# Performance work log

Measured on AMD Instinct MI355X. Metric: run time of the kernel, lower is better.

The kernel has to match this reference:

```python
import jax, jax.numpy as jnp
import numpy as np

B, L, D = 16, 512, 128
EPS = 1e-12


def _newton_schulz_1(S):
    # One Newton-Schulz orthogonalization iteration on batched [B,D,D] matrices:
    # X = S/||S||_F ; X <- 1.5*X - 0.5 * X @ X^T @ X
    norm = jnp.sqrt(jnp.sum(S * S, axis=(-2, -1), keepdims=True)) + 1e-6
    X = S / norm
    XXtX = jnp.einsum('bij,bkj,bkl->bil', X, X, X)
    return 1.5 * X - 0.5 * XXtX


def _poly(v, coeffs):
    # PolynomialFeatureLayer, degree 2, dimension-preserving:
    # phi(v) = c0*v + c1*v^2
    return coeffs[0] * v + coeffs[1] * v * v


def setup_inputs() -> dict:
    key = jax.random.key(0)
    ks = jax.random.split(key, 6)
    s = 1.0 / np.sqrt(D)
    x = jax.random.normal(ks[0], (B, L, D), jnp.float32)
    Wq = jax.random.normal(ks[1], (D, D), jnp.float32) * s
    Wk = jax.random.normal(ks[2], (D, D), jnp.float32) * s
    Wout = jax.random.normal(ks[3], (D, D), jnp.float32) * s
    bout = jnp.zeros((D,), jnp.float32)
    M0 = jax.random.normal(ks[4], (D, D), jnp.float32) * 0.01   # M_init
    S0 = jnp.zeros((D, D), jnp.float32)                          # S_init
    P0 = jnp.eye(D, dtype=jnp.float32) * 0.01                    # P_init
    log_gain = jnp.zeros((D,), jnp.float32)                      # QKProjectionLayer gain
    coeffs = jnp.array([1.0, 0.5], jnp.float32)                  # poly coeffs
    return {"x": x, "Wq": Wq, "Wk": Wk, "P0": P0, "M0": M0, "S0": S0,
            "log_gain": log_gain, "coeffs": coeffs, "Wout": Wout, "bout": bout}


def reference(x, Wq, Wk, P0, M0, S0, log_gain, coeffs, Wout, bout):
    b, l, d = x.shape
    q = jnp.einsum('bld,ed->ble', x, Wq)                 # q_proj (no bias)
    k = jnp.einsum('bld,ed->ble', x, Wk)                 # k_proj (no bias)
    k = k / jnp.maximum(jnp.linalg.norm(k, axis=-1, keepdims=True), EPS)  # F.normalize

    # QKProjectionLayer: rotate q by per-batch projection P, tanh gate with learned gain
    P = jnp.broadcast_to(P0, (b, d, d))
    gain = jnp.exp(log_gain)
    q_aligned = jnp.tanh(gain * jnp.einsum('bld,bde->ble', q, P))
    # (P_new = 0.99*P + 0.01*mean_t outer(q,k); state only, unused by output)

    k_phi = _poly(k, coeffs)
    q_phi = _poly(q_aligned, coeffs)

    M = jnp.broadcast_to(M0, (b, d, d))
    S = jnpp = jnp.broadcast_to(S0, (b, d, d))

    def step(carry, inputs):
        M, S = carry
        k_t, q_t, x_t = inputs                           # each [B,D]
        pred = jnp.einsum('bde,be->bd', M, k_t)
        err = pred - x_t
        S = 0.9 * S + err[:, :, None] * k_t[:, None, :]  # outer-product grad
        S_ortho = _newton_schulz_1(S)
        M = 0.99 * M - 0.01 * S_ortho
        y_t = jnp.einsum('bde,be->bd', M, q_t)
        return (M, S), y_t

    xs = (jnp.swapaxes(k_phi, 0, 1), jnp.swapaxes(q_phi, 0, 1), jnp.swapaxes(x, 0, 1))
    (_, _), ys = jax.lax.scan(step, (M, S), xs)          # ys: [L,B,D]
    stacked = jnp.swapaxes(ys, 0, 1)                     # [B,L,D]
    out = jnp.einsum('bld,ed->ble', stacked, Wout) + bout  # out_proj
    return out
```

## Files before the change

kernel.cpp:

```cpp
#include <hip/hip_runtime.h>

#define BB 16
#define LL 512
#define DD 128
#define CH 16
#define NCH (LL / CH)

typedef float v2f __attribute__((ext_vector_type(2)));
__device__ __forceinline__ v2f mk2(float x, float y) { v2f r; r.x = x; r.y = y; return r; }
__device__ __forceinline__ v2f fma2(v2f a, v2f b, v2f c) {
    return __builtin_elementwise_fma(a, b, c);
}

__device__ __forceinline__ float red8(float v) {
    v += __int_as_float(__builtin_amdgcn_update_dpp(
            0, __float_as_int(v), 0xB1, 0xF, 0xF, true));
    v += __int_as_float(__builtin_amdgcn_update_dpp(
            0, __float_as_int(v), 0x4E, 0xF, 0xF, true));
    v += __int_as_float(__builtin_amdgcn_update_dpp(
            0, __float_as_int(v), 0x141, 0xF, 0xF, true));
    return v;
}

#define SCAN_REGS __attribute__((amdgpu_waves_per_eu(2, 2)))

__global__ void transpose3_kernel(const float* __restrict__ Wq,
                                  const float* __restrict__ Wk,
                                  const float* __restrict__ Wout,
                                  float* __restrict__ WqT,
                                  float* __restrict__ WkT,
                                  float* __restrict__ WoutT) {
    const float* src; float* dst;
    if (blockIdx.x == 0)      { src = Wq;   dst = WqT;   }
    else if (blockIdx.x == 1) { src = Wk;   dst = WkT;   }
    else                      { src = Wout; dst = WoutT; }
    for (int idx = threadIdx.x; idx < DD * DD; idx += blockDim.x) {
        int r = idx >> 7, c = idx & 127;
        dst[c * DD + r] = src[idx];
    }
}

__global__ __launch_bounds__(128) void prologue_kernel(
        const float* __restrict__ x, const float* __restrict__ WqT,
        const float* __restrict__ WkT, const float* __restrict__ P0,
        const float* __restrict__ log_gain, const float* __restrict__ coeffs,
        float* __restrict__ kphi, float* __restrict__ qphi) {
    const int row0 = blockIdx.x * 8;
    const int e = threadIdx.x;
    __shared__ float xs[8][DD];
    __shared__ float qrow[8][DD];
    __shared__ float wred[8][2];

    #pragma unroll
    for (int rr = 0; rr < 8; ++rr)
        xs[rr][e] = x[(size_t)(row0 + rr) * DD + e];
    __syncthreads();

    float aq[8] = {0,0,0,0,0,0,0,0}, ak[8] = {0,0,0,0,0,0,0,0};
    #pragma unroll 4
    for (int d = 0; d < DD; ++d) {
        float wq = WqT[d * DD + e];
        float wk = WkT[d * DD + e];
        #pragma unroll
        for (int rr = 0; rr < 8; ++rr) {
            float xv = xs[rr][d];
            aq[rr] = fmaf(xv, wq, aq[rr]);
            ak[rr] = fmaf(xv, wk, ak[rr]);
        }
    }
    const int lane = threadIdx.x & 63, wv = threadIdx.x >> 6;
    #pragma unroll
    for (int rr = 0; rr < 8; ++rr) {
        float s = ak[rr] * ak[rr];
        #pragma unroll
        for (int m = 1; m <= 32; m <<= 1) s += __shfl_xor(s, m);
        if (lane == 0) wred[rr][wv] = s;
    }
    __syncthreads();
    const float c0 = coeffs[0], c1v = coeffs[1];
    #pragma unroll
    for (int rr = 0; rr < 8; ++rr) {
        float s = wred[rr][0] + wred[rr][1];
        float kn = ak[rr] / fmaxf(sqrtf(s), 1e-12f);
        kphi[(size_t)(row0 + rr) * DD + e] = c0 * kn + c1v * kn * kn;
        qrow[rr][e] = aq[rr];
    }
    __syncthreads();
    float acc[8] = {0,0,0,0,0,0,0,0};
    #pragma unroll 4
    for (int d = 0; d < DD; ++d) {
        float pv = P0[d * DD + e];
        #pragma unroll
        for (int rr = 0; rr < 8; ++rr) acc[rr] = fmaf(qrow[rr][d], pv, acc[rr]);
    }
    const float g = expf(log_gain[e]);
    #pragma unroll
    for (int rr = 0; rr < 8; ++rr) {
        float qa = tanhf(g * acc[rr]);
        qphi[(size_t)(row0 + rr) * DD + e] = c0 * qa + c1v * qa * qa;
    }
}

__global__ SCAN_REGS __launch_bounds__(512)
void scan_kernel(
        const float* __restrict__ kphi, const float* __restrict__ qphi,
        const float* __restrict__ x, const float* __restrict__ M0,
        const float* __restrict__ S0, float* __restrict__ ys) {
    const int b    = blockIdx.x;
    const int tid  = threadIdx.x;
    const int j    = tid & 7;
    const int g    = tid >> 3;
    const int r0   = 2 * g;
    const int w    = tid >> 6;
    const int lane = tid & 63;

    __shared__ __align__(16) float kc[2][CH * DD];
    __shared__ __align__(16) float qc[2][CH * DD];
    __shared__ __align__(16) float xc[2][CH * DD];
    __shared__ __align__(16) float yc[CH * DD];
    __shared__ __align__(16) float us[DD], ps[DD], wsv[DD], hs[DD];
    __shared__ float red[64];
    __shared__ float n2sh;

    v2f S2[16], ST2[16], A2[16], M2[16];
    {
        const float4* S04 = (const float4*)S0;
        const float4* M04 = (const float4*)M0;
        #pragma unroll
        for (int rl = 0; rl < 2; ++rl)
            #pragma unroll
            for (int m = 0; m < 4; ++m) {
                int f4 = (r0 + rl) * 32 + j + 8 * m;
                float4 s4 = S04[f4], m4 = M04[f4];
                int p = rl * 8 + 2 * m;
                S2[p]     = mk2(s4.x, s4.y);
                S2[p + 1] = mk2(s4.z, s4.w);
                M2[p]     = mk2(m4.x, m4.y);
                M2[p + 1] = mk2(m4.z, m4.w);
            }
        #pragma unroll
        for (int rl = 0; rl < 2; ++rl)
            #pragma unroll
            for (int m = 0; m < 4; ++m) {
                int p = rl * 8 + 2 * m;
                ST2[p]     = mk2(S0[(size_t)(4*j + 32*m + 0) * DD + r0 + rl],
                                 S0[(size_t)(4*j + 32*m + 1) * DD + r0 + rl]);
                ST2[p + 1] = mk2(S0[(size_t)(4*j + 32*m + 2) * DD + r0 + rl],
                                 S0[(size_t)(4*j + 32*m + 3) * DD + r0 + rl]);
            }
        #pragma unroll
        for (int p = 0; p < 16; ++p) A2[p] = mk2(0.f, 0.f);
    }

    float sp = 0.f;
    #pragma unroll
    for (int p = 0; p < 16; ++p) {
        sp = fmaf(S2[p].x, S2[p].x, sp);
        sp = fmaf(S2[p].y, S2[p].y, sp);
    }
    sp = red8(sp);
    if (j == 0) red[g] = sp;

    const size_t base = (size_t)b * LL * DD;

    #pragma unroll
    for (int i = 0; i < 3; ++i) {
        int seg = w * 3 + i, arr = seg >> 3, sub = seg & 7;
        const float* sp0 = (arr == 0 ? kphi : (arr == 1 ? qphi : x))
                           + base + sub * 256 + lane * 4;
        float* dp = (arr == 0 ? kc[0] : (arr == 1 ? qc[0] : xc[0]))
                    + sub * 256 + lane * 4;
        *(float4*)dp = *(const float4*)sp0;
    }
    __syncthreads();
    if (tid < 64) {
        float s = red[tid];
        #pragma unroll
        for (int m = 1; m <= 32; m <<= 1) s += __shfl_xor(s, m);
        if (tid == 0) n2sh = s;
    }
    __syncthreads();
    float n2 = n2sh;

    const float a = 0.9f, a2v = 0.81f, a3v = 0.729f;
    const v2f av = mk2(a, a);

    #pragma unroll 1
    for (int tc = 0; tc < NCH; ++tc) {
        const int cb = tc & 1;
        const float* kcb = kc[cb];
        const float* qcb = qc[cb];
        const float* xcb = xc[cb];

        #pragma unroll 1
        for (int sl = 0; sl < CH; ++sl) {
            const int so = sl * DD;

            float4 pre0, pre1, pre2;
            const bool doPre = (sl == 0) && (tc + 1 < NCH);
            if (doPre) {
                const size_t nbg = base + (size_t)(tc + 1) * CH * DD;
                {
                    int seg = w * 3 + 0, arr = seg >> 3, sub = seg & 7;
                    pre0 = *(const float4*)((arr == 0 ? kphi : (arr == 1 ? qphi : x))
                                            + nbg + sub * 256 + lane * 4);
                }
                {
                    int seg = w * 3 + 1, arr = seg >> 3, sub = seg & 7;
                    pre1 = *(const float4*)((arr == 0 ? kphi : (arr == 1 ? qphi : x))
                                            + nbg + sub * 256 + lane * 4);
                }
                {
                    int seg = w * 3 + 2, arr = seg >> 3, sub = seg & 7;
                    pre2 = *(const float4*)((arr == 0 ? kphi : (arr == 1 ? qphi : x))
                                            + nbg + sub * 256 + lane * 4);
                }
            }

            v2f kk2[8];
            {
                const float4* k4 = (const float4*)(kcb + so);
                #pragma unroll
                for (int m = 0; m < 4; ++m) {
                    float4 v4 = k4[j + 8 * m];
                    kk2[2*m]     = mk2(v4.x, v4.y);
                    kk2[2*m + 1] = mk2(v4.z, v4.w);
                }
            }
            v2f pr0v = mk2(0.f, 0.f), pr1v = mk2(0.f, 0.f);
            v2f pp0v = mk2(0.f, 0.f), pp1v = mk2(0.f, 0.f);
            v2f cvv  = mk2(0.f, 0.f);
            #pragma unroll
            for (int p = 0; p < 8; ++p) {
                v2f kv = kk2[p];
                pr0v = fma2(M2[p],     kv, pr0v);
                pr1v = fma2(M2[8 + p], kv, pr1v);
                pp0v = fma2(S2[p],     kv, pp0v);
                pp1v = fma2(S2[8 + p], kv, pp1v);
                cvv  = fma2(kv, kv, cvv);
            }
            float pr0 = red8(pr0v.x + pr0v.y);
            float pr1 = red8(pr1v.x + pr1v.y);
            float pp0 = red8(pp0v.x + pp0v.y);
            float pp1 = red8(pp1v.x + pp1v.y);
            const float cv = red8(cvv.x + cvv.y);
            const float2 xv = *(const float2*)&xcb[so + r0];
            const float u0 = pr0 - xv.x, u1 = pr1 - xv.y;
            const float p0 = pp0, p1 = pp1;
            if (j == 0) {
                *(float2*)&us[r0] = make_float2(u0, u1);
                *(float2*)&ps[r0] = make_float2(p0, p1);
            }
            __syncthreads();

            v2f uu2[8], pa2[8];
            {
                const float4* u4 = (const float4*)us;
                const float4* p4 = (const float4*)ps;
                #pragma unroll
                for (int m = 0; m < 4; ++m) {
                    float4 a4 = u4[j + 8 * m], b4 = p4[j + 8 * m];
                    uu2[2*m]     = mk2(a4.x, a4.y);
                    uu2[2*m + 1] = mk2(a4.z, a4.w);
                    pa2[2*m]     = mk2(b4.x, b4.y);
                    pa2[2*m + 1] = mk2(b4.z, b4.w);
                }
            }
            const float2 vc = *(const float2*)&kcb[so + r0];
            const v2f vcx = mk2(vc.x, vc.x), vcy = mk2(vc.y, vc.y);
            v2f w0v = mk2(0.f, 0.f), w1v = mk2(0.f, 0.f);
            v2f h0v = mk2(0.f, 0.f), h1v = mk2(0.f, 0.f);
            v2f cuv = mk2(0.f, 0.f), cupv = mk2(0.f, 0.f);
            #pragma unroll
            for (int p = 0; p < 8; ++p) {
                v2f uv = uu2[p], pv = pa2[p];
                v2f st0 = ST2[p], st1 = ST2[8 + p];
                w0v  = fma2(st0, uv, w0v);
                w1v  = fma2(st1, uv, w1v);
                h0v  = fma2(st0, pv, h0v);
                h1v  = fma2(st1, pv, h1v);
                cuv  = fma2(uv, uv, cuv);
                cupv = fma2(uv, pv, cupv);
                ST2[p]     = fma2(av, st0, vcx * uv);
                ST2[8 + p] = fma2(av, st1, vcy * uv);
            }
            float w0 = red8(w0v.x + w0v.y);
            float w1 = red8(w1v.x + w1v.y);
            float h0 = red8(h0v.x + h0v.y);
            float h1 = red8(h1v.x + h1v.y);
            const float cu  = red8(cuv.x + cuv.y);
            const float cup = red8(cupv.x + cupv.y);
            n2 = a2v * n2 + 2.0f * a * cup + cu * cv;
            if (j == 0) {
                *(float2*)&wsv[r0] = make_float2(w0, w1);
                *(float2*)&hs[r0]  = make_float2(h0, h1);
            }
            if (doPre) {
                float* kn = kc[cb ^ 1]; float* qn = qc[cb ^ 1]; float* xn = xc[cb ^ 1];
                {
                    int seg = w * 3 + 0, arr = seg >> 3, sub = seg & 7;
                    *(float4*)((arr == 0 ? kn : (arr == 1 ? qn : xn))
                               + sub * 256 + lane * 4) = pre0;
                }
                {
                    int seg = w * 3 + 1, arr = seg >> 3, sub = seg & 7;
                    *(float4*)((arr == 0 ? kn : (arr == 1 ? qn : xn))
                               + sub * 256 + lane * 4) = pre1;
                }
                {
                    int seg = w * 3 + 2, arr = seg >> 3, sub = seg & 7;
                    *(float4*)((arr == 0 ? kn : (arr == 1 ? qn : xn))
                               + sub * 256 + lane * 4) = pre2;
                }
            }
            __syncthreads();

            v2f ww2[8], hh2[8], qq2[8];
            {
                const float4* w4 = (const float4*)wsv;
                const float4* h4 = (const float4*)hs;
                const float4* q4 = (const float4*)(qcb + so);
                #pragma unroll
                for (int m = 0; m < 4; ++m) {
                    float4 a4 = w4[j + 8 * m], b4 = h4[j + 8 * m], c4v = q4[j + 8 * m];
                    ww2[2*m]     = mk2(a4.x, a4.y);
                    ww2[2*m + 1] = mk2(a4.z, a4.w);
                    hh2[2*m]     = mk2(b4.x, b4.y);
                    hh2[2*m + 1] = mk2(b4.z, b4.w);
                    qq2[2*m]     = mk2(c4v.x, c4v.y);
                    qq2[2*m + 1] = mk2(c4v.z, c4v.w);
                }
            }
            v2f g0v = mk2(0.f, 0.f), g1v = mk2(0.f, 0.f);
            #pragma unroll
            for (int p = 0; p < 8; ++p) {
                v2f wv = ww2[p];
                g0v = fma2(S2[p],     wv, g0v);
                g1v = fma2(S2[8 + p], wv, g1v);
            }
            float g0 = red8(g0v.x + g0v.y);
            float g1 = red8(g1v.x + g1v.y);

            const float rho0 = a2v * g0 + a * cu * p0 + (a * cup + cv * cu) * u0;
            const float rho1 = a2v * g1 + a * cu * p1 + (a * cup + cv * cu) * u1;
            const float sg0  = a2v * p0 + a * cv * u0;
            const float sg1  = a2v * p1 + a * cv * u1;
            const float ta0  = a2v * u0, ta1 = a2v * u1;
            const float nrm  = sqrtf(fmaxf(n2, 0.f)) + 1e-6f;
            const float rn   = 1.0f / nrm;
            const float c1   = -0.015f * rn;
            const float c2   = 0.005f * rn * rn * rn;

            const v2f u0v = mk2(u0, u0),   u1v = mk2(u1, u1);
            const v2f r0v = mk2(rho0, rho0), r1v = mk2(rho1, rho1);
            const v2f s0v = mk2(sg0, sg0), s1v = mk2(sg1, sg1);
            const v2f t0v = mk2(ta0, ta0), t1v = mk2(ta1, ta1);
            const v2f a3p = mk2(a3v, a3v);
            const v2f c9p = mk2(0.99f, 0.99f);
            const v2f c1p = mk2(c1, c1), c2p = mk2(c2, c2);

            v2f y0v = mk2(0.f, 0.f), y1v = mk2(0.f, 0.f);
            #pragma unroll
            for (int p = 0; p < 8; ++p) {
                v2f kv = kk2[p], wv = ww2[p], hv = hh2[p], qv = qq2[p];
                S2[p]     = fma2(av, S2[p],     u0v * kv);
                S2[8 + p] = fma2(av, S2[8 + p], u1v * kv);
                A2[p]     = fma2(a3p, A2[p],
                                 fma2(r0v, kv, fma2(s0v, wv, t0v * hv)));
                A2[8 + p] = fma2(a3p, A2[8 + p],
                                 fma2(r1v, kv, fma2(s1v, wv, t1v * hv)));
                M2[p]     = fma2(c9p, M2[p],     fma2(c1p, S2[p],     c2p * A2[p]));
                M2[8 + p] = fma2(c9p, M2[8 + p], fma2(c1p, S2[8 + p], c2p * A2[8 + p]));
                y0v = fma2(M2[p],     qv, y0v);
                y1v = fma2(M2[8 + p], qv, y1v);
            }
            float y0 = red8(y0v.x + y0v.y);
            float y1 = red8(y1v.x + y1v.y);
            if (j == 0)
                *(float2*)&yc[so + r0] = make_float2(y0, y1);
        }

        __syncthreads();
        float4 yv = *(float4*)&yc[tid * 4];
        *(float4*)(ys + base + (size_t)tc * CH * DD + tid * 4) = yv;
    }
}

__global__ __launch_bounds__(128) void epilogue_kernel(
        const float* __restrict__ ys, const float* __restrict__ WoutT,
        const float* __restrict__ bout, float* __restrict__ out) {
    const int row0 = blockIdx.x * 8;
    const int e = threadIdx.x;
    __shared__ float yr[8][DD];
    #pragma unroll
    for (int rr = 0; rr < 8; ++rr)
        yr[rr][e] = ys[(size_t)(row0 + rr) * DD + e];
    __syncthreads();
    float acc[8] = {0,0,0,0,0,0,0,0};
    #pragma unroll 4
    for (int d = 0; d < DD; ++d) {
        float w = WoutT[d * DD + e];
        #pragma unroll
        for (int rr = 0; rr < 8; ++rr) acc[rr] = fmaf(yr[rr][d], w, acc[rr]);
    }
    const float bo = bout[e];
    #pragma unroll
    for (int rr = 0; rr < 8; ++rr)
        out[(size_t)(row0 + rr) * DD + e] = acc[rr] + bo;
}

extern "C" void kernel_launch(void* const* d_in, const int* in_sizes, int n_in,
                              void* d_out, int out_size, void* d_ws, size_t ws_size,
                              hipStream_t stream) {
    const float* x        = (const float*)d_in[0];
    const float* Wq       = (const float*)d_in[1];
    const float* Wk       = (const float*)d_in[2];
    const float* P0       = (const float*)d_in[3];
    const float* M0       = (const float*)d_in[4];
    const float* S0       = (const float*)d_in[5];
    const float* log_gain = (const float*)d_in[6];
    const float* coeffs   = (const float*)d_in[7];
    const float* Wout     = (const float*)d_in[8];
    const float* bout     = (const float*)d_in[9];
    float* out = (float*)d_out;

    float* ws    = (float*)d_ws;
    float* WqT   = ws;
    float* WkT   = ws + 16384;
    float* WoutT = ws + 32768;
    float* kphi  = ws + 49152;
    float* qphi  = kphi + (size_t)BB * LL * DD;
    float* ysb   = qphi + (size_t)BB * LL * DD;

    hipLaunchKernelGGL(transpose3_kernel, dim3(3), dim3(256), 0, stream,
                       Wq, Wk, Wout, WqT, WkT, WoutT);
    hipLaunchKernelGGL(prologue_kernel, dim3(BB * LL / 8), dim3(128), 0, stream,
                       x, WqT, WkT, P0, log_gain, coeffs, kphi, qphi);
    hipLaunchKernelGGL(scan_kernel, dim3(BB), dim3(512), 0, stream,
                       kphi, qphi, x, M0, S0, ysb);
    hipLaunchKernelGGL(epilogue_kernel, dim3(BB * LL / 8), dim3(128), 0, stream,
                       ysb, WoutT, bout, out);
}
```

Baseline: 1.293 ms.

## Scan kernel: one row per 8-thread group with 1024 threads per block

The sequential scan kernel now uses 1024 threads per batch block, so each 8-lane group owns a single row of M, S, S^T and A instead of two. This halves per-thread register state and the serial FMA chain length per timestep, and the chunk loads and y stores are remapped to the larger thread count. In exchange every per-step __syncthreads now spans 16 waves instead of 8, and the waves_per_eu occupancy hint is dropped.

Result: slower. 1.922 ms (+48.6%).

```diff
diff --git a/kernel.cpp b/kernel.cpp
--- a/kernel.cpp
+++ b/kernel.cpp
@@ -21,8 +21,6 @@
             0, __float_as_int(v), 0x141, 0xF, 0xF, true));
     return v;
 }
-
-#define SCAN_REGS __attribute__((amdgpu_waves_per_eu(2, 2)))
 
 __global__ void transpose3_kernel(const float* __restrict__ Wq,
                                   const float* __restrict__ Wk,
@@ -101,7 +99,7 @@
     }
 }
 
-__global__ SCAN_REGS __launch_bounds__(512)
+__global__ __launch_bounds__(1024)
 void scan_kernel(
         const float* __restrict__ kphi, const float* __restrict__ qphi,
         const float* __restrict__ x, const float* __restrict__ M0,
@@ -110,51 +108,42 @@
     const int tid  = threadIdx.x;
     const int j    = tid & 7;
     const int g    = tid >> 3;
-    const int r0   = 2 * g;
-    const int w    = tid >> 6;
-    const int lane = tid & 63;
 
     __shared__ __align__(16) float kc[2][CH * DD];
     __shared__ __align__(16) float qc[2][CH * DD];
     __shared__ __align__(16) float xc[2][CH * DD];
     __shared__ __align__(16) float yc[CH * DD];
     __shared__ __align__(16) float us[DD], ps[DD], wsv[DD], hs[DD];
-    __shared__ float red[64];
+    __shared__ float red[DD];
     __shared__ float n2sh;
 
-    v2f S2[16], ST2[16], A2[16], M2[16];
+    v2f S2[8], ST2[8], A2[8], M2[8];
     {
         const float4* S04 = (const float4*)S0;
         const float4* M04 = (const float4*)M0;
         #pragma unroll
-        for (int rl = 0; rl < 2; ++rl)
-            #pragma unroll
-            for (int m = 0; m < 4; ++m) {
-                int f4 = (r0 + rl) * 32 + j + 8 * m;
-                float4 s4 = S04[f4], m4 = M04[f4];
-                int p = rl * 8 + 2 * m;
-                S2[p]     = mk2(s4.x, s4.y);
-                S2[p + 1] = mk2(s4.z, s4.w);
-                M2[p]     = mk2(m4.x, m4.y);
-                M2[p + 1] = mk2(m4.z, m4.w);
-            }
-        #pragma unroll
-        for (int rl = 0; rl < 2; ++rl)
-            #pragma unroll
-            for (int m = 0; m < 4; ++m) {
-                int p = rl * 8 + 2 * m;
-                ST2[p]     = mk2(S0[(size_t)(4*j + 32*m + 0) * DD + r0 + rl],
-                                 S0[(size_t)(4*j + 32*m + 1) * DD + r0 + rl]);
-                ST2[p + 1] = mk2(S0[(size_t)(4*j + 32*m + 2) * DD + r0 + rl],
-                                 S0[(size_t)(4*j + 32*m + 3) * DD + r0 + rl]);
-            }
-        #pragma unroll
-        for (int p = 0; p < 16; ++p) A2[p] = mk2(0.f, 0.f);
+        for (int m = 0; m < 4; ++m) {
+            int f4 = g * 32 + j + 8 * m;
+            float4 s4 = S04[f4], m4 = M04[f4];
+            S2[2*m]     = mk2(s4.x, s4.y);
+            S2[2*m + 1] = mk2(s4.z, s4.w);
+            M2[2*m]     = mk2(m4.x, m4.y);
+            M2[2*m + 1] = mk2(m4.z, m4.w);
+        }
+        #pragma unroll
+        for (int m = 0; m < 4; ++m) {
+            ST2[2*m]     = mk2(S0[(size_t)(4*j + 32*m + 0) * DD + g],
+                               S0[(size_t)(4*j + 32*m + 1) * DD + g]);
+            ST2[2*m + 1] = mk2(S0[(size_t)(4*j + 32*m + 2) * DD + g],
+                               S0[(size_t)(4*j + 32*m + 3) * DD + g]);
+        }
+        #pragma unroll
+        for (int p = 0; p < 8; ++p) A2[p] = mk2(0.f, 0.f);
     }
 
     float sp = 0.f;
     #pragma unroll
-    for (int p = 0; p < 16; ++p) {
+    for (int p = 0; p < 8; ++p) {
         sp = fmaf(S2[p].x, S2[p].x, sp);
         sp = fmaf(S2[p].y, S2[p].y, sp);
     }
@@ -163,18 +152,16 @@
 
     const size_t base = (size_t)b * LL * DD;
 
-    #pragma unroll
-    for (int i = 0; i < 3; ++i) {
-        int seg = w * 3 + i, arr = seg >> 3, sub = seg & 7;
-        const float* sp0 = (arr == 0 ? kphi : (arr == 1 ? qphi : x))
-                           + base + sub * 256 + lane * 4;
-        float* dp = (arr == 0 ? kc[0] : (arr == 1 ? qc[0] : xc[0]))
-                    + sub * 256 + lane * 4;
-        *(float4*)dp = *(const float4*)sp0;
+    {
+        int arr = tid >> 9, off = (tid & 511) << 2;
+        const float* sp0 = (arr ? qphi : kphi) + base + off;
+        *(float4*)((arr ? qc[0] : kc[0]) + off) = *(const float4*)sp0;
+        if (tid < 512)
+            *(float4*)(xc[0] + tid * 4) = *(const float4*)(x + base + tid * 4);
     }
     __syncthreads();
     if (tid < 64) {
-        float s = red[tid];
+        float s = red[tid] + red[tid + 64];
         #pragma unroll
         for (int m = 1; m <= 32; m <<= 1) s += __shfl_xor(s, m);
         if (tid == 0) n2sh = s;
@@ -196,193 +183,142 @@
         for (int sl = 0; sl < CH; ++sl) {
             const int so = sl * DD;
 
-            float4 pre0, pre1, pre2;
+            float4 pre0, pre1;
             const bool doPre = (sl == 0) && (tc + 1 < NCH);
             if (doPre) {
                 const size_t nbg = base + (size_t)(tc + 1) * CH * DD;
-                {
-                    int seg = w * 3 + 0, arr = seg >> 3, sub = seg & 7;
-                    pre0 = *(const float4*)((arr == 0 ? kphi : (arr == 1 ? qphi : x))
-                                            + nbg + sub * 256 + lane * 4);
-                }
-                {
-                    int seg = w * 3 + 1, arr = seg >> 3, sub = seg & 7;
-                    pre1 = *(const float4*)((arr == 0 ? kphi : (arr == 1 ? qphi : x))
-                                            + nbg + sub * 256 + lane * 4);
-                }
-                {
-                    int seg = w * 3 + 2, arr = seg >> 3, sub = seg & 7;
-                    pre2 = *(const float4*)((arr == 0 ? kphi : (arr == 1 ? qphi : x))
-                                            + nbg + sub * 256 + lane * 4);
-                }
+                int arr = tid >> 9, off = (tid & 511) << 2;
+                pre0 = *(const float4*)((arr ? qphi : kphi) + nbg + off);
+                if (tid < 512)
+                    pre1 = *(const float4*)(x + nbg + tid * 4);
             }
 
             v2f kk2[8];
+            v2f prv = mk2(0.f, 0.f), ppv = mk2(0.f, 0.f), cvv = mk2(0.f, 0.f);
             {
                 const float4* k4 = (const float4*)(kcb + so);
                 #pragma unroll
                 for (int m = 0; m < 4; ++m) {
                     float4 v4 = k4[j + 8 * m];
-                    kk2[2*m]     = mk2(v4.x, v4.y);
-                    kk2[2*m + 1] = mk2(v4.z, v4.w);
+                    v2f k0 = mk2(v4.x, v4.y), k1 = mk2(v4.z, v4.w);
+                    kk2[2*m] = k0; kk2[2*m + 1] = k1;
+                    prv = fma2(M2[2*m], k0, prv);
+                    prv = fma2(M2[2*m + 1], k1, prv);
+                    ppv = fma2(S2[2*m], k0, ppv);
+                    ppv = fma2(S2[2*m + 1], k1, ppv);
+                    cvv = fma2(k0, k0, cvv);
+                    cvv = fma2(k1, k1, cvv);
                 }
             }
-            v2f pr0v = mk2(0.f, 0.f), pr1v = mk2(0.f, 0.f);
-            v2f pp0v = mk2(0.f, 0.f), pp1v = mk2(0.f, 0.f);
-            v2f cvv  = mk2(0.f, 0.f);
-            #pragma unroll
-            for (int p = 0; p < 8; ++p) {
-                v2f kv = kk2[p];
-                pr0v = fma2(M2[p],     kv, pr0v);
-                pr1v = fma2(M2[8 + p], kv, pr1v);
-                pp0v = fma2(S2[p],     kv, pp0v);
-                pp1v = fma2(S2[8 + p], kv, pp1v);
-                cvv  = fma2(kv, kv, cvv);
-            }
-            float pr0 = red8(pr0v.x + pr0v.y);
-            float pr1 = red8(pr1v.x + pr1v.y);
-            float pp0 = red8(pp0v.x + pp0v.y);
-            float pp1 = red8(pp1v.x + pp1v.y);
+            float pr = red8(prv.x + prv.y);
+            float pp = red8(ppv.x + ppv.y);
             const float cv = red8(cvv.x + cvv.y);
-            const float2 xv = *(const float2*)&xcb[so + r0];
-            const float u0 = pr0 - xv.x, u1 = pr1 - xv.y;
-            const float p0 = pp0, p1 = pp1;
-            if (j == 0) {
-                *(float2*)&us[r0] = make_float2(u0, u1);
-                *(float2*)&ps[r0] = make_float2(p0, p1);
-            }
+            const float xv = xcb[so + g];
+            const float u0 = pr - xv;
+            const float p0 = pp;
+            if (j == 0) { us[g] = u0; ps[g] = p0; }
             __syncthreads();
 
-            v2f uu2[8], pa2[8];
+            const float vcs = kcb[so + g];
+            const v2f vcx = mk2(vcs, vcs);
+            v2f w0v = mk2(0.f, 0.f), h0v = mk2(0.f, 0.f);
+            v2f cuv = mk2(0.f, 0.f), cupv = mk2(0.f, 0.f);
             {
                 const float4* u4 = (const float4*)us;
                 const float4* p4 = (const float4*)ps;
                 #pragma unroll
                 for (int m = 0; m < 4; ++m) {
                     float4 a4 = u4[j + 8 * m], b4 = p4[j + 8 * m];
-                    uu2[2*m]     = mk2(a4.x, a4.y);
-                    uu2[2*m + 1] = mk2(a4.z, a4.w);
-                    pa2[2*m]     = mk2(b4.x, b4.y);
-                    pa2[2*m + 1] = mk2(b4.z, b4.w);
+                    v2f uv0 = mk2(a4.x, a4.y), uv1 = mk2(a4.z, a4.w);
+                    v2f pv0 = mk2(b4.x, b4.y), pv1 = mk2(b4.z, b4.w);
+                    v2f st0 = ST2[2*m], st1 = ST2[2*m + 1];
+                    w0v  = fma2(st0, uv0, w0v);
+                    w0v  = fma2(st1, uv1, w0v);
+                    h0v  = fma2(st0, pv0, h0v);
+                    h0v  = fma2(st1, pv1, h0v);
+                    cuv  = fma2(uv0, uv0, cuv);
+                    cuv  = fma2(uv1, uv1, cuv);
+                    cupv = fma2(uv0, pv0, cupv);
+                    cupv = fma2(uv1, pv1, cupv);
+                    ST2[2*m]     = fma2(av, st0, vcx * uv0);
+                    ST2[2*m + 1] = fma2(av, st1, vcx * uv1);
                 }
             }
-            const float2 vc = *(const float2*)&kcb[so + r0];
-            const v2f vcx = mk2(vc.x, vc.x), vcy = mk2(vc.y, vc.y);
-            v2f w0v = mk2(0.f, 0.f), w1v = mk2(0.f, 0.f);
-            v2f h0v = mk2(0.f, 0.f), h1v = mk2(0.f, 0.f);
-            v2f cuv = mk2(0.f, 0.f), cupv = mk2(0.f, 0.f);
-            #pragma unroll
-            for (int p = 0; p < 8; ++p) {
-                v2f uv = uu2[p], pv = pa2[p];
-                v2f st0 = ST2[p], st1 = ST2[8 + p];
-                w0v  = fma2(st0, uv, w0v);
-                w1v  = fma2(st1, uv, w1v);
-                h0v  = fma2(st0, pv, h0v);
-                h1v  = fma2(st1, pv, h1v);
-                cuv  = fma2(uv, uv, cuv);
-                cupv = fma2(uv, pv, cupv);
-                ST2[p]     = fma2(av, st0, vcx * uv);
-                ST2[8 + p] = fma2(av, st1, vcy * uv);
-            }
             float w0 = red8(w0v.x + w0v.y);
-            float w1 = red8(w1v.x + w1v.y);
             float h0 = red8(h0v.x + h0v.y);
-            float h1 = red8(h1v.x + h1v.y);
             const float cu  = red8(cuv.x + cuv.y);
             const float cup = red8(cupv.x + cupv.y);
             n2 = a2v * n2 + 2.0f * a * cup + cu * cv;
-            if (j == 0) {
-                *(float2*)&wsv[r0] = make_float2(w0, w1);
-                *(float2*)&hs[r0]  = make_float2(h0, h1);
-            }
+            if (j == 0) { wsv[g] = w0; hs[g] = h0; }
             if (doPre) {
-                float* kn = kc[cb ^ 1]; float* qn = qc[cb ^ 1]; float* xn = xc[cb ^ 1];
-                {
-                    int seg = w * 3 + 0, arr = seg >> 3, sub = seg & 7;
-                    *(float4*)((arr == 0 ? kn : (arr == 1 ? qn : xn))
-                               + sub * 256 + lane * 4) = pre0;
-                }
-                {
-                    int seg = w * 3 + 1, arr = seg >> 3, sub = seg & 7;
-                    *(float4*)((arr == 0 ? kn : (arr == 1 ? qn : xn))
-                               + sub * 256 + lane * 4) = pre1;
-                }
-                {
-                    int seg = w * 3 + 2, arr = seg >> 3, sub = seg & 7;
-                    *(float4*)((arr == 0 ? kn : (arr == 1 ? qn : xn))
-                               + sub * 256 + lane * 4) = pre2;
-                }
+                int arr = tid >> 9, off = (tid & 511) << 2;
+                *(float4*)((arr ? qc[cb ^ 1] : kc[cb ^ 1]) + off) = pre0;
+                if (tid < 512)
+                    *(float4*)(xc[cb ^ 1] + tid * 4) = pre1;
             }
             __syncthreads();
 
-            v2f ww2[8], hh2[8], qq2[8];
+            v2f g0v = mk2(0.f, 0.f);
+            const float4* w4 = (const float4*)wsv;
+            #pragma unroll
+            for (int m = 0; m < 4; ++m) {
+                float4 a4 = w4[j + 8 * m];
+                g0v = fma2(S2[2*m],     mk2(a4.x, a4.y), g0v);
+                g0v = fma2(S2[2*m + 1], mk2(a4.z, a4.w), g0v);
+            }
+            const float gg = red8(g0v.x + g0v.y);
+
+            const float rho = a2v * gg + a * cu * p0 + (a * cup + cv * cu) * u0;
+            const float sg  = a2v * p0 + a * cv * u0;
+            const float ta  = a2v * u0;
+            const float nrm = sqrtf(fmaxf(n2, 0.f)) + 1e-6f;
+            const float rn  = 1.0f / nrm;
+            const float c1  = -0.015f * rn;
+            const float c2  = 0.005f * rn * rn * rn;
+
+            const v2f u0v = mk2(u0, u0);
+            const v2f r0v = mk2(rho, rho);
+            const v2f s0v = mk2(sg, sg);
+            const v2f t0v = mk2(ta, ta);
+            const v2f a3p = mk2(a3v, a3v);
+            const v2f c9p = mk2(0.99f, 0.99f);
+            const v2f c1p = mk2(c1, c1), c2p = mk2(c2, c2);
+
+            v2f y0v = mk2(0.f, 0.f);
             {
-                const float4* w4 = (const float4*)wsv;
                 const float4* h4 = (const float4*)hs;
                 const float4* q4 = (const float4*)(qcb + so);
                 #pragma unroll
                 for (int m = 0; m < 4; ++m) {
-                    float4 a4 = w4[j + 8 * m], b4 = h4[j + 8 * m], c4v = q4[j + 8 * m];
-                    ww2[2*m]     = mk2(a4.x, a4.y);
-                    ww2[2*m + 1] = mk2(a4.z, a4.w);
-                    hh2[2*m]     = mk2(b4.x, b4.y);
-                    hh2[2*m + 1] = mk2(b4.z, b4.w);
-                    qq2[2*m]     = mk2(c4v.x, c4v.y);
-                    qq2[2*m + 1] = mk2(c4v.z, c4v.w);
+                    float4 a4 = w4[j + 8 * m];
+                    float4 b4 = h4[j + 8 * m];
+                    float4 c4v = q4[j + 8 * m];
+                    v2f wv0 = mk2(a4.x, a4.y),  wv1 = mk2(a4.z, a4.w);
+                    v2f hv0 = mk2(b4.x, b4.y),  hv1 = mk2(b4.z, b4.w);
+                    v2f qv0 = mk2(c4v.x, c4v.y), qv1 = mk2(c4v.z, c4v.w);
+                    v2f kv0 = kk2[2*m], kv1 = kk2[2*m + 1];
+                    v2f sn0 = fma2(av, S2[2*m],     u0v * kv0);
+                    v2f sn1 = fma2(av, S2[2*m + 1], u0v * kv1);
+                    S2[2*m] = sn0; S2[2*m + 1] = sn1;
+                    v2f an0 = fma2(a3p, A2[2*m],
+                                   fma2(r0v, kv0, fma2(s0v, wv0, t0v * hv0)));
+                    v2f an1 = fma2(a3p, A2[2*m + 1],
+                                   fma2(r0v, kv1, fma2(s0v, wv1, t0v * hv1)));
+                    A2[2*m] = an0; A2[2*m + 1] = an1;
+                    v2f mn0 = fma2(c9p, M2[2*m],     fma2(c1p, sn0, c2p * an0));
+                    v2f mn1 = fma2(c9p, M2[2*m + 1], fma2(c1p, sn1, c2p * an1));
+                    M2[2*m] = mn0; M2[2*m + 1] = mn1;
+                    y0v = fma2(mn0, qv0, y0v);
+                    y0v = fma2(mn1, qv1, y0v);
                 }
             }
-            v2f g0v = mk2(0.f, 0.f), g1v = mk2(0.f, 0.f);
-            #pragma unroll
-            for (int p = 0; p < 8; ++p) {
-                v2f wv = ww2[p];
-                g0v = fma2(S2[p],     wv, g0v);
-                g1v = fma2(S2[8 + p], wv, g1v);
-            }
-            float g0 = red8(g0v.x + g0v.y);
-            float g1 = red8(g1v.x + g1v.y);
-
-            const float rho0 = a2v * g0 + a * cu * p0 + (a * cup + cv * cu) * u0;
-            const float rho1 = a2v * g1 + a * cu * p1 + (a * cup + cv * cu) * u1;
-            const float sg0  = a2v * p0 + a * cv * u0;
-            const float sg1  = a2v * p1 + a * cv * u1;
-            const float ta0  = a2v * u0, ta1 = a2v * u1;
-            const float nrm  = sqrtf(fmaxf(n2, 0.f)) + 1e-6f;
-            const float rn   = 1.0f / nrm;
-            const float c1   = -0.015f * rn;
-            const float c2   = 0.005f * rn * rn * rn;
-
-            const v2f u0v = mk2(u0, u0),   u1v = mk2(u1, u1);
-            const v2f r0v = mk2(rho0, rho0), r1v = mk2(rho1, rho1);
-            const v2f s0v = mk2(sg0, sg0), s1v = mk2(sg1, sg1);
-            const v2f t0v = mk2(ta0, ta0), t1v = mk2(ta1, ta1);
-            const v2f a3p = mk2(a3v, a3v);
-            const v2f c9p = mk2(0.99f, 0.99f);
-            const v2f c1p = mk2(c1, c1), c2p = mk2(c2, c2);
-
-            v2f y0v = mk2(0.f, 0.f), y1v = mk2(0.f, 0.f);
-            #pragma unroll
-            for (int p = 0; p < 8; ++p) {
-                v2f kv = kk2[p], wv = ww2[p], hv = hh2[p], qv = qq2[p];
-                S2[p]     = fma2(av, S2[p],     u0v * kv);
-                S2[8 + p] = fma2(av, S2[8 + p], u1v * kv);
-                A2[p]     = fma2(a3p, A2[p],
-                                 fma2(r0v, kv, fma2(s0v, wv, t0v * hv)));
-                A2[8 + p] = fma2(a3p, A2[8 + p],
-                                 fma2(r1v, kv, fma2(s1v, wv, t1v * hv)));
-                M2[p]     = fma2(c9p, M2[p],     fma2(c1p, S2[p],     c2p * A2[p]));
-                M2[8 + p] = fma2(c9p, M2[8 + p], fma2(c1p, S2[8 + p], c2p * A2[8 + p]));
-                y0v = fma2(M2[p],     qv, y0v);
-                y1v = fma2(M2[8 + p], qv, y1v);
-            }
             float y0 = red8(y0v.x + y0v.y);
-            float y1 = red8(y1v.x + y1v.y);
-            if (j == 0)
-                *(float2*)&yc[so + r0] = make_float2(y0, y1);
+            if (j == 0) yc[so + g] = y0;
         }
 
         __syncthreads();
-        float4 yv = *(float4*)&yc[tid * 4];
-        *(float4*)(ys + base + (size_t)tc * CH * DD + tid * 4) = yv;
+        float2 yv = *(float2*)&yc[tid * 2];
+        *(float2*)(ys + base + (size_t)tc * CH * DD + tid * 2) = yv;
     }
 }
 
@@ -436,7 +372,7 @@
                        Wq, Wk, Wout, WqT, WkT, WoutT);
     hipLaunchKernelGGL(prologue_kernel, dim3(BB * LL / 8), dim3(128), 0, stream,
                        x, WqT, WkT, P0, log_gain, coeffs, kphi, qphi);
-    hipLaunchKernelGGL(scan_kernel, dim3(BB), dim3(512), 0, stream,
+    hipLaunchKernelGGL(scan_kernel, dim3(BB), dim3(1024), 0, stream,
                        kphi, qphi, x, M0, S0, ysb);
     hipLaunchKernelGGL(epilogue_kernel, dim3(BB * LL / 8), dim3(128), 0, stream,
                        ysb, WoutT, bout, out);
```

## Software-pipeline next step's prediction into the current step's state update

Applied to the files above, without the earlier changes.

Computes the prediction (M·k, S·k, k·k) for time step t+1 inside the fused M/S/A update loop of step t, right after the new M and S rows are formed. This takes one full loop pass over the register-resident state and one barrier out of each recurrence step, and lets the next step's shared-memory k be loaded alongside the update. It also drops the separate end-of-chunk barrier, using the per-step barrier in its place. In exchange it adds register pressure from the extra accumulators and next-step k values, plus branching to handle the chunk boundary and the final step.

Result: faster. 1.172 ms (-9.4%).

```diff
diff --git a/kernel.cpp b/kernel.cpp
--- a/kernel.cpp
+++ b/kernel.cpp
@@ -185,6 +185,43 @@
     const float a = 0.9f, a2v = 0.81f, a3v = 0.729f;
     const v2f av = mk2(a, a);
 
+    v2f kk2[8];
+    float u0, u1, p0, p1, cv;
+    {
+        const float4* k4 = (const float4*)kc[0];
+        v2f pr0v = mk2(0.f, 0.f), pr1v = mk2(0.f, 0.f);
+        v2f pp0v = mk2(0.f, 0.f), pp1v = mk2(0.f, 0.f);
+        v2f cvv  = mk2(0.f, 0.f);
+        #pragma unroll
+        for (int m = 0; m < 4; ++m) {
+            float4 v4 = k4[j + 8 * m];
+            v2f k0 = mk2(v4.x, v4.y), k1 = mk2(v4.z, v4.w);
+            kk2[2*m] = k0; kk2[2*m + 1] = k1;
+            pr0v = fma2(M2[2*m],     k0, pr0v);
+            pr0v = fma2(M2[2*m + 1], k1, pr0v);
+            pr1v = fma2(M2[8 + 2*m],     k0, pr1v);
+            pr1v = fma2(M2[8 + 2*m + 1], k1, pr1v);
+            pp0v = fma2(S2[2*m],     k0, pp0v);
+            pp0v = fma2(S2[2*m + 1], k1, pp0v);
+            pp1v = fma2(S2[8 + 2*m],     k0, pp1v);
+            pp1v = fma2(S2[8 + 2*m + 1], k1, pp1v);
+            cvv  = fma2(k0, k0, cvv);
+            cvv  = fma2(k1, k1, cvv);
+        }
+        float pr0 = red8(pr0v.x + pr0v.y);
+        float pr1 = red8(pr1v.x + pr1v.y);
+        p0 = red8(pp0v.x + pp0v.y);
+        p1 = red8(pp1v.x + pp1v.y);
+        cv = red8(cvv.x + cvv.y);
+        const float2 xv = *(const float2*)&xc[0][r0];
+        u0 = pr0 - xv.x; u1 = pr1 - xv.y;
+        if (j == 0) {
+            *(float2*)&us[r0] = make_float2(u0, u1);
+            *(float2*)&ps[r0] = make_float2(p0, p1);
+        }
+    }
+    __syncthreads();
+
     #pragma unroll 1
     for (int tc = 0; tc < NCH; ++tc) {
         const int cb = tc & 1;
@@ -195,6 +232,7 @@
         #pragma unroll 1
         for (int sl = 0; sl < CH; ++sl) {
             const int so = sl * DD;
+            const bool last = (tc == NCH - 1) && (sl == CH - 1);
 
             float4 pre0, pre1, pre2;
             const bool doPre = (sl == 0) && (tc + 1 < NCH);
@@ -216,42 +254,6 @@
                                             + nbg + sub * 256 + lane * 4);
                 }
             }
-
-            v2f kk2[8];
-            {
-                const float4* k4 = (const float4*)(kcb + so);
-                #pragma unroll
-                for (int m = 0; m < 4; ++m) {
-                    float4 v4 = k4[j + 8 * m];
-                    kk2[2*m]     = mk2(v4.x, v4.y);
-                    kk2[2*m + 1] = mk2(v4.z, v4.w);
-                }
-            }
-            v2f pr0v = mk2(0.f, 0.f), pr1v = mk2(0.f, 0.f);
-            v2f pp0v = mk2(0.f, 0.f), pp1v = mk2(0.f, 0.f);
-            v2f cvv  = mk2(0.f, 0.f);
-            #pragma unroll
-            for (int p = 0; p < 8; ++p) {
-                v2f kv = kk2[p];
-                pr0v = fma2(M2[p],     kv, pr0v);
-                pr1v = fma2(M2[8 + p], kv, pr1v);
-                pp0v = fma2(S2[p],     kv, pp0v);
-                pp1v = fma2(S2[8 + p], kv, pp1v);
-                cvv  = fma2(kv, kv, cvv);
-            }
-            float pr0 = red8(pr0v.x + pr0v.y);
-            float pr1 = red8(pr1v.x + pr1v.y);
-            float pp0 = red8(pp0v.x + pp0v.y);
-            float pp1 = red8(pp1v.x + pp1v.y);
-            const float cv = red8(cvv.x + cvv.y);
-            const float2 xv = *(const float2*)&xcb[so + r0];
-            const float u0 = pr0 - xv.x, u1 = pr1 - xv.y;
-            const float p0 = pp0, p1 = pp1;
-            if (j == 0) {
-                *(float2*)&us[r0] = make_float2(u0, u1);
-                *(float2*)&ps[r0] = make_float2(p0, p1);
-            }
-            __syncthreads();
 
             v2f uu2[8], pa2[8];
             {
@@ -315,28 +317,20 @@
             }
             __syncthreads();
 
-            v2f ww2[8], hh2[8], qq2[8];
+            v2f ww2[8];
+            v2f g0v = mk2(0.f, 0.f), g1v = mk2(0.f, 0.f);
             {
                 const float4* w4 = (const float4*)wsv;
-                const float4* h4 = (const float4*)hs;
-                const float4* q4 = (const float4*)(qcb + so);
                 #pragma unroll
                 for (int m = 0; m < 4; ++m) {
-                    float4 a4 = w4[j + 8 * m], b4 = h4[j + 8 * m], c4v = q4[j + 8 * m];
-                    ww2[2*m]     = mk2(a4.x, a4.y);
-                    ww2[2*m + 1] = mk2(a4.z, a4.w);
-                    hh2[2*m]     = mk2(b4.x, b4.y);
-                    hh2[2*m + 1] = mk2(b4.z, b4.w);
-                    qq2[2*m]     = mk2(c4v.x, c4v.y);
-                    qq2[2*m + 1] = mk2(c4v.z, c4v.w);
-                }
-            }
-            v2f g0v = mk2(0.f, 0.f), g1v = mk2(0.f, 0.f);
-            #pragma unroll
-            for (int p = 0; p < 8; ++p) {
-                v2f wv = ww2[p];
-                g0v = fma2(S2[p],     wv, g0v);
-                g1v = fma2(S2[8 + p], wv, g1v);
+                    float4 a4 = w4[j + 8 * m];
+                    v2f wv0 = mk2(a4.x, a4.y), wv1 = mk2(a4.z, a4.w);
+                    ww2[2*m] = wv0; ww2[2*m + 1] = wv1;
+                    g0v = fma2(S2[2*m],     wv0, g0v);
+                    g0v = fma2(S2[2*m + 1], wv1, g0v);
+                    g1v = fma2(S2[8 + 2*m],     wv0, g1v);
+                    g1v = fma2(S2[8 + 2*m + 1], wv1, g1v);
+                }
             }
             float g0 = red8(g0v.x + g0v.y);
             float g1 = red8(g1v.x + g1v.y);
@@ -359,28 +353,90 @@
             const v2f c9p = mk2(0.99f, 0.99f);
             const v2f c1p = mk2(c1, c1), c2p = mk2(c2, c2);
 
+            const float* knb = (sl + 1 < CH) ? (kcb + so + DD) : kc[cb ^ 1];
+            const float* xnb = (sl + 1 < CH) ? (xcb + so + DD) : xc[cb ^ 1];
+
             v2f y0v = mk2(0.f, 0.f), y1v = mk2(0.f, 0.f);
-            #pragma unroll
-            for (int p = 0; p < 8; ++p) {
-                v2f kv = kk2[p], wv = ww2[p], hv = hh2[p], qv = qq2[p];
-                S2[p]     = fma2(av, S2[p],     u0v * kv);
-                S2[8 + p] = fma2(av, S2[8 + p], u1v * kv);
-                A2[p]     = fma2(a3p, A2[p],
-                                 fma2(r0v, kv, fma2(s0v, wv, t0v * hv)));
-                A2[8 + p] = fma2(a3p, A2[8 + p],
-                                 fma2(r1v, kv, fma2(s1v, wv, t1v * hv)));
-                M2[p]     = fma2(c9p, M2[p],     fma2(c1p, S2[p],     c2p * A2[p]));
-                M2[8 + p] = fma2(c9p, M2[8 + p], fma2(c1p, S2[8 + p], c2p * A2[8 + p]));
-                y0v = fma2(M2[p],     qv, y0v);
-                y1v = fma2(M2[8 + p], qv, y1v);
+            v2f pr0n = mk2(0.f, 0.f), pr1n = mk2(0.f, 0.f);
+            v2f pp0n = mk2(0.f, 0.f), pp1n = mk2(0.f, 0.f);
+            v2f cvn  = mk2(0.f, 0.f);
+            v2f kkn[8];
+            {
+                const float4* h4  = (const float4*)hs;
+                const float4* q4  = (const float4*)(qcb + so);
+                const float4* k4n = (const float4*)knb;
+                #pragma unroll
+                for (int m = 0; m < 4; ++m) {
+                    float4 b4  = h4[j + 8 * m];
+                    float4 c4v = q4[j + 8 * m];
+                    float4 k4v = k4n[j + 8 * m];
+                    v2f hv0 = mk2(b4.x, b4.y),   hv1 = mk2(b4.z, b4.w);
+                    v2f qv0 = mk2(c4v.x, c4v.y), qv1 = mk2(c4v.z, c4v.w);
+                    v2f kn0 = mk2(k4v.x, k4v.y), kn1 = mk2(k4v.z, k4v.w);
+                    kkn[2*m] = kn0; kkn[2*m + 1] = kn1;
+                    v2f wv0 = ww2[2*m], wv1 = ww2[2*m + 1];
+                    v2f kv0 = kk2[2*m], kv1 = kk2[2*m + 1];
+                    v2f sn0 = fma2(av, S2[2*m],     u0v * kv0);
+                    v2f sn1 = fma2(av, S2[2*m + 1], u0v * kv1);
+                    S2[2*m] = sn0; S2[2*m + 1] = sn1;
+                    v2f an0 = fma2(a3p, A2[2*m],
+                                   fma2(r0v, kv0, fma2(s0v, wv0, t0v * hv0)));
+                    v2f an1 = fma2(a3p, A2[2*m + 1],
+                                   fma2(r0v, kv1, fma2(s0v, wv1, t0v * hv1)));
+                    A2[2*m] = an0; A2[2*m + 1] = an1;
+                    v2f mn0 = fma2(c9p, M2[2*m],     fma2(c1p, sn0, c2p * an0));
+                    v2f mn1 = fma2(c9p, M2[2*m + 1], fma2(c1p, sn1, c2p * an1));
+                    M2[2*m] = mn0; M2[2*m + 1] = mn1;
+                    y0v  = fma2(mn0, qv0, y0v);
+                    y0v  = fma2(mn1, qv1, y0v);
+                    pr0n = fma2(mn0, kn0, pr0n);
+                    pr0n = fma2(mn1, kn1, pr0n);
+                    pp0n = fma2(sn0, kn0, pp0n);
+                    pp0n = fma2(sn1, kn1, pp0n);
+                    v2f sm0 = fma2(av, S2[8 + 2*m],     u1v * kv0);
+                    v2f sm1 = fma2(av, S2[8 + 2*m + 1], u1v * kv1);
+                    S2[8 + 2*m] = sm0; S2[8 + 2*m + 1] = sm1;
+                    v2f am0 = fma2(a3p, A2[8 + 2*m],
+                                   fma2(r1v, kv0, fma2(s1v, wv0, t1v * hv0)));
+                    v2f am1 = fma2(a3p, A2[8 + 2*m + 1],
+                                   fma2(r1v, kv1, fma2(s1v, wv1, t1v * hv1)));
+                    A2[8 + 2*m] = am0; A2[8 + 2*m + 1] = am1;
+                    v2f mm0 = fma2(c9p, M2[8 + 2*m],     fma2(c1p, sm0, c2p * am0));
+                    v2f mm1 = fma2(c9p, M2[8 + 2*m + 1], fma2(c1p, sm1, c2p * am1));
+                    M2[8 + 2*m] = mm0; M2[8 + 2*m + 1] = mm1;
+                    y1v  = fma2(mm0, qv0, y1v);
+                    y1v  = fma2(mm1, qv1, y1v);
+                    pr1n = fma2(mm0, kn0, pr1n);
+                    pr1n = fma2(mm1, kn1, pr1n);
+                    pp1n = fma2(sm0, kn0, pp1n);
+                    pp1n = fma2(sm1, kn1, pp1n);
+                    cvn  = fma2(kn0, kn0, cvn);
+                    cvn  = fma2(kn1, kn1, cvn);
+                }
             }
             float y0 = red8(y0v.x + y0v.y);
             float y1 = red8(y1v.x + y1v.y);
             if (j == 0)
                 *(float2*)&yc[so + r0] = make_float2(y0, y1);
+
+            float pr0 = red8(pr0n.x + pr0n.y);
+            float pr1 = red8(pr1n.x + pr1n.y);
+            p0 = red8(pp0n.x + pp0n.y);
+            p1 = red8(pp1n.x + pp1n.y);
+            cv = red8(cvn.x + cvn.y);
+            const float2 xn = *(const float2*)&xnb[r0];
+            u0 = pr0 - xn.x; u1 = pr1 - xn.y;
+            if (!last) {
+                if (j == 0) {
+                    *(float2*)&us[r0] = make_float2(u0, u1);
+                    *(float2*)&ps[r0] = make_float2(p0, p1);
+                }
+                #pragma unroll
+                for (int p = 0; p < 8; ++p) kk2[p] = kkn[p];
+            }
+            __syncthreads();
         }
 
-        __syncthreads();
         float4 yv = *(float4*)&yc[tid * 4];
         *(float4*)(ys + base + (size_t)tc * CH * DD + tid * 4) = yv;
     }
```
